# Kernel tuning notes

Hardware: AMD Instinct MI355X
Metric: run time of the kernel (lower is better)

Reference implementation:

```python
import jax, jax.numpy as jnp
import numpy as np

D_K = 64

def setup_inputs() -> dict:
    key = jax.random.key(0)
    k1, k2, k3 = jax.random.split(key, 3)
    shape = (4, 16, 2048, D_K)  # [batch, heads, seq, d_k]
    return {
        "q": jax.random.normal(k1, shape, dtype=jnp.float32),
        "k": jax.random.normal(k2, shape, dtype=jnp.float32),
        "v": jax.random.normal(k3, shape, dtype=jnp.float32),
    }

def reference(q, k, v):
    # scores: [B, H, S, S] = Q K^T / sqrt(d_k)
    scale = 1.0 / jnp.sqrt(jnp.asarray(D_K, dtype=q.dtype))
    scores = jnp.einsum("bhqd,bhkd->bhqk", q, k) * scale
    attn = jax.nn.softmax(scores, axis=-1)
    out = jnp.einsum("bhqk,bhkd->bhqd", attn, v)
    return out
```

## Files before the change

### kernel.cpp

```cpp
#include <hip/hip_runtime.h>


#define S_LEN 2048
#define D_K 64
#define BQ 256
#define BK 64
#define NT (S_LEN / BK)
#define LST 68

typedef __attribute__((ext_vector_type(8))) _Float16 fragh;
typedef __attribute__((ext_vector_type(4))) _Float16 half4v;
typedef __attribute__((ext_vector_type(2))) _Float16 half2v;
typedef __attribute__((ext_vector_type(16))) float f32x16;
typedef __attribute__((ext_vector_type(2))) unsigned int uint2v;
typedef __attribute__((ext_vector_type(4))) unsigned int uint4v;

__device__ __forceinline__ half2v pkrtz(float a, float b) {
  return __builtin_bit_cast(half2v, __builtin_amdgcn_cvt_pkrtz(a, b));
}
__device__ __forceinline__ half4v pk4(float a, float b, float c, float d) {
  return __builtin_shufflevector(pkrtz(a, b), pkrtz(c, d), 0, 1, 2, 3);
}
__device__ __forceinline__ fragh ldfrag(const _Float16* p) {
  half4v lo = *(const half4v*)p;
  half4v hv = *(const half4v*)(p + 4);
  return __builtin_shufflevector(lo, hv, 0, 1, 2, 3, 4, 5, 6, 7);
}

__global__ __launch_bounds__(512, 2) void sdpa_kernel(
    const float* __restrict__ q, const float* __restrict__ k,
    const float* __restrict__ v, float* __restrict__ out) {
  __shared__ _Float16 Ks[2][BK][LST];
  __shared__ _Float16 Vs[2][D_K][LST];

  const int t = threadIdx.x;
  const int wave = t >> 6;
  const int lane = t & 63;
  const int ln = lane & 31;
  const int hi = lane >> 5;

  const int blk = blockIdx.x;
  const int bh = (blk & 7) * 8 + (blk >> 6);
  const int q0 = ((blk >> 3) & 7) * BQ;

  const float* qp = q + ((size_t)bh * S_LEN + q0 + wave * 32) * D_K;
  const float* kp = k + (size_t)bh * S_LEN * D_K;
  const float* vp = v + (size_t)bh * S_LEN * D_K;

  const float qs = 0.125f * 1.44269504088896340736f;

  fragh qf[4];
  #pragma unroll
  for (int ks = 0; ks < 4; ++ks) {
    const float* src = qp + ln * D_K + ks * 16 + hi * 8;
    float4 a = *(const float4*)src;
    float4 b = *(const float4*)(src + 4);
    half4v lo = pk4(a.x * qs, a.y * qs, a.z * qs, a.w * qs);
    half4v hv = pk4(b.x * qs, b.y * qs, b.z * qs, b.w * qs);
    qf[ks] = __builtin_shufflevector(lo, hv, 0, 1, 2, 3, 4, 5, 6, 7);
  }

  const int pr = t & 31;
  const int dg = t >> 5;

  float4 kpre[2], vpre[2];
  {
    #pragma unroll
    for (int i = 0; i < 2; ++i) kpre[i] = *(const float4*)(kp + i * 2048 + t * 4);
    const float* vs0 = vp + 2 * pr * D_K + dg * 4;
    vpre[0] = *(const float4*)(vs0);
    vpre[1] = *(const float4*)(vs0 + D_K);
  }

  f32x16 O[2];
  #pragma unroll
  for (int dt = 0; dt < 2; ++dt)
    #pragma unroll
    for (int r = 0; r < 16; ++r) O[dt][r] = 0.f;
  float lsum = 0.f;

  #pragma unroll 2
  for (int kt = 0; kt < NT; ++kt) {
    const int bb = kt & 1;

    #pragma unroll
    for (int i = 0; i < 2; ++i) {
      int e = i * 2048 + t * 4;
      *(half4v*)&Ks[bb][e >> 6][e & 63] =
          pk4(kpre[i].x, kpre[i].y, kpre[i].z, kpre[i].w);
    }
    {
      int vd = dg * 4, vc = 2 * pr;
      *(half2v*)&Vs[bb][vd + 0][vc] = pkrtz(vpre[0].x, vpre[1].x);
      *(half2v*)&Vs[bb][vd + 1][vc] = pkrtz(vpre[0].y, vpre[1].y);
      *(half2v*)&Vs[bb][vd + 2][vc] = pkrtz(vpre[0].z, vpre[1].z);
      *(half2v*)&Vs[bb][vd + 3][vc] = pkrtz(vpre[0].w, vpre[1].w);
    }
    if (kt + 1 < NT) {
      const float* kb = kp + (kt + 1) * (BK * D_K);
      const float* vb = vp + (kt + 1) * (BK * D_K);
      #pragma unroll
      for (int i = 0; i < 2; ++i) kpre[i] = *(const float4*)(kb + i * 2048 + t * 4);
      const float* vs0 = vb + 2 * pr * D_K + dg * 4;
      vpre[0] = *(const float4*)(vs0);
      vpre[1] = *(const float4*)(vs0 + D_K);
    }
    __syncthreads();

    f32x16 sx[2];
    #pragma unroll
    for (int kt32 = 0; kt32 < 2; ++kt32) {
      fragh kf[4];
      #pragma unroll
      for (int ks = 0; ks < 4; ++ks)
        kf[ks] = ldfrag(&Ks[bb][kt32 * 32 + ln][ks * 16 + hi * 8]);
      f32x16 s;
      #pragma unroll
      for (int r = 0; r < 16; ++r) s[r] = 0.f;
      __builtin_amdgcn_s_setprio(1);
      #pragma unroll
      for (int ks = 0; ks < 4; ++ks)
        s = __builtin_amdgcn_mfma_f32_32x32x16_f16(kf[ks], qf[ks], s, 0, 0, 0);
      __builtin_amdgcn_s_setprio(0);
      sx[kt32] = s;
    }

    #pragma unroll
    for (int kt32 = 0; kt32 < 2; ++kt32) {
      fragh vf[2][2];
      #pragma unroll
      for (int ks16 = 0; ks16 < 2; ++ks16)
        #pragma unroll
        for (int dt = 0; dt < 2; ++dt)
          vf[ks16][dt] =
              ldfrag(&Vs[bb][dt * 32 + ln][kt32 * 32 + ks16 * 16 + hi * 8]);

      float p[16];
      #pragma unroll
      for (int r = 0; r < 16; ++r) p[r] = __builtin_amdgcn_exp2f(sx[kt32][r]);
      float t0 = (p[0] + p[1]) + (p[2] + p[3]);
      float t1 = (p[4] + p[5]) + (p[6] + p[7]);
      float t2 = (p[8] + p[9]) + (p[10] + p[11]);
      float t3 = (p[12] + p[13]) + (p[14] + p[15]);
      lsum += (t0 + t1) + (t2 + t3);

      unsigned w[8];
      #pragma unroll
      for (int i2 = 0; i2 < 8; ++i2)
        w[i2] = __builtin_bit_cast(unsigned, pkrtz(p[2 * i2], p[2 * i2 + 1]));
      uint2v a0 = __builtin_amdgcn_permlane32_swap(w[0], w[2], false, false);
      uint2v a1 = __builtin_amdgcn_permlane32_swap(w[1], w[3], false, false);
      uint2v a2 = __builtin_amdgcn_permlane32_swap(w[4], w[6], false, false);
      uint2v a3 = __builtin_amdgcn_permlane32_swap(w[5], w[7], false, false);
      uint4v f0 = {a0.x, a1.x, a0.y, a1.y};
      uint4v f1 = {a2.x, a3.x, a2.y, a3.y};
      fragh pf0 = __builtin_bit_cast(fragh, f0);
      fragh pf1 = __builtin_bit_cast(fragh, f1);

      __builtin_amdgcn_s_setprio(1);
      #pragma unroll
      for (int dt = 0; dt < 2; ++dt) {
        O[dt] = __builtin_amdgcn_mfma_f32_32x32x16_f16(vf[0][dt], pf0,
                                                       O[dt], 0, 0, 0);
        O[dt] = __builtin_amdgcn_mfma_f32_32x32x16_f16(vf[1][dt], pf1,
                                                       O[dt], 0, 0, 0);
      }
      __builtin_amdgcn_s_setprio(0);
    }
  }

  {
    float l = lsum + __shfl_xor(lsum, 32, 64);
    float inv = __builtin_amdgcn_rcpf(l);
    float* ob = out + ((size_t)bh * S_LEN + q0 + wave * 32 + ln) * D_K;
    #pragma unroll
    for (int dt = 0; dt < 2; ++dt) {
      #pragma unroll
      for (int g = 0; g < 4; ++g) {
        float4 o4;
        o4.x = O[dt][4 * g + 0] * inv;
        o4.y = O[dt][4 * g + 1] * inv;
        o4.z = O[dt][4 * g + 2] * inv;
        o4.w = O[dt][4 * g + 3] * inv;
        *(float4*)&ob[dt * 32 + g * 8 + hi * 4] = o4;
      }
    }
  }
}

extern "C" void kernel_launch(void* const* d_in, const int* in_sizes, int n_in,
                              void* d_out, int out_size, void* d_ws, size_t ws_size,
                              hipStream_t stream) {
  const float* q = (const float*)d_in[0];
  const float* k = (const float*)d_in[1];
  const float* v = (const float*)d_in[2];
  float* out = (float*)d_out;
  dim3 grid((S_LEN / BQ) * 64);
  dim3 block(512);
  sdpa_kernel<<<grid, block, 0, stream>>>(q, k, v, out);
}
```

Measured before the change: 191.9 us.

## Software-pipeline PV MFMA one tile behind QK with triple-buffered V

```diff
diff --git a/kernel.cpp b/kernel.cpp
--- a/kernel.cpp
+++ b/kernel.cpp
@@ -31,7 +31,7 @@
     const float* __restrict__ q, const float* __restrict__ k,
     const float* __restrict__ v, float* __restrict__ out) {
   __shared__ _Float16 Ks[2][BK][LST];
-  __shared__ _Float16 Vs[2][D_K][LST];
+  __shared__ _Float16 Vs[3][D_K][LST];
 
   const int t = threadIdx.x;
   const int wave = t >> 6;
@@ -79,7 +79,14 @@
     for (int r = 0; r < 16; ++r) O[dt][r] = 0.f;
   float lsum = 0.f;
 
-  #pragma unroll 2
+  fragh pz;
+  #pragma unroll
+  for (int j = 0; j < 8; ++j) pz[j] = (_Float16)0.f;
+  fragh pp00 = pz, pp01 = pz, pp10 = pz, pp11 = pz;
+
+  int vt = 0;
+  int pvt = 2;
+
   for (int kt = 0; kt < NT; ++kt) {
     const int bb = kt & 1;
 
@@ -91,10 +98,10 @@
     }
     {
       int vd = dg * 4, vc = 2 * pr;
-      *(half2v*)&Vs[bb][vd + 0][vc] = pkrtz(vpre[0].x, vpre[1].x);
-      *(half2v*)&Vs[bb][vd + 1][vc] = pkrtz(vpre[0].y, vpre[1].y);
-      *(half2v*)&Vs[bb][vd + 2][vc] = pkrtz(vpre[0].z, vpre[1].z);
-      *(half2v*)&Vs[bb][vd + 3][vc] = pkrtz(vpre[0].w, vpre[1].w);
+      *(half2v*)&Vs[vt][vd + 0][vc] = pkrtz(vpre[0].x, vpre[1].x);
+      *(half2v*)&Vs[vt][vd + 1][vc] = pkrtz(vpre[0].y, vpre[1].y);
+      *(half2v*)&Vs[vt][vd + 2][vc] = pkrtz(vpre[0].z, vpre[1].z);
+      *(half2v*)&Vs[vt][vd + 3][vc] = pkrtz(vpre[0].w, vpre[1].w);
     }
     if (kt + 1 < NT) {
       const float* kb = kp + (kt + 1) * (BK * D_K);
@@ -107,13 +114,12 @@
     }
     __syncthreads();
 
-    f32x16 sx[2];
-    #pragma unroll
-    for (int kt32 = 0; kt32 < 2; ++kt32) {
+    f32x16 sx0, sx1;
+    {
       fragh kf[4];
       #pragma unroll
       for (int ks = 0; ks < 4; ++ks)
-        kf[ks] = ldfrag(&Ks[bb][kt32 * 32 + ln][ks * 16 + hi * 8]);
+        kf[ks] = ldfrag(&Ks[bb][0 * 32 + ln][ks * 16 + hi * 8]);
       f32x16 s;
       #pragma unroll
       for (int r = 0; r < 16; ++r) s[r] = 0.f;
@@ -122,28 +128,34 @@
       for (int ks = 0; ks < 4; ++ks)
         s = __builtin_amdgcn_mfma_f32_32x32x16_f16(kf[ks], qf[ks], s, 0, 0, 0);
       __builtin_amdgcn_s_setprio(0);
-      sx[kt32] = s;
-    }
-
-    #pragma unroll
-    for (int kt32 = 0; kt32 < 2; ++kt32) {
-      fragh vf[2][2];
-      #pragma unroll
-      for (int ks16 = 0; ks16 < 2; ++ks16)
-        #pragma unroll
-        for (int dt = 0; dt < 2; ++dt)
-          vf[ks16][dt] =
-              ldfrag(&Vs[bb][dt * 32 + ln][kt32 * 32 + ks16 * 16 + hi * 8]);
-
+      sx0 = s;
+    }
+    {
+      fragh kf[4];
+      #pragma unroll
+      for (int ks = 0; ks < 4; ++ks)
+        kf[ks] = ldfrag(&Ks[bb][1 * 32 + ln][ks * 16 + hi * 8]);
+      f32x16 s;
+      #pragma unroll
+      for (int r = 0; r < 16; ++r) s[r] = 0.f;
+      __builtin_amdgcn_s_setprio(1);
+      #pragma unroll
+      for (int ks = 0; ks < 4; ++ks)
+        s = __builtin_amdgcn_mfma_f32_32x32x16_f16(kf[ks], qf[ks], s, 0, 0, 0);
+      __builtin_amdgcn_s_setprio(0);
+      sx1 = s;
+    }
+
+    fragh pn00, pn01, pn10, pn11;
+    {
       float p[16];
       #pragma unroll
-      for (int r = 0; r < 16; ++r) p[r] = __builtin_amdgcn_exp2f(sx[kt32][r]);
+      for (int r = 0; r < 16; ++r) p[r] = __builtin_amdgcn_exp2f(sx0[r]);
       float t0 = (p[0] + p[1]) + (p[2] + p[3]);
       float t1 = (p[4] + p[5]) + (p[6] + p[7]);
       float t2 = (p[8] + p[9]) + (p[10] + p[11]);
       float t3 = (p[12] + p[13]) + (p[14] + p[15]);
       lsum += (t0 + t1) + (t2 + t3);
-
       unsigned w[8];
       #pragma unroll
       for (int i2 = 0; i2 < 8; ++i2)
@@ -154,18 +166,81 @@
       uint2v a3 = __builtin_amdgcn_permlane32_swap(w[5], w[7], false, false);
       uint4v f0 = {a0.x, a1.x, a0.y, a1.y};
       uint4v f1 = {a2.x, a3.x, a2.y, a3.y};
-      fragh pf0 = __builtin_bit_cast(fragh, f0);
-      fragh pf1 = __builtin_bit_cast(fragh, f1);
-
-      __builtin_amdgcn_s_setprio(1);
-      #pragma unroll
-      for (int dt = 0; dt < 2; ++dt) {
-        O[dt] = __builtin_amdgcn_mfma_f32_32x32x16_f16(vf[0][dt], pf0,
-                                                       O[dt], 0, 0, 0);
-        O[dt] = __builtin_amdgcn_mfma_f32_32x32x16_f16(vf[1][dt], pf1,
-                                                       O[dt], 0, 0, 0);
-      }
-      __builtin_amdgcn_s_setprio(0);
+      pn00 = __builtin_bit_cast(fragh, f0);
+      pn01 = __builtin_bit_cast(fragh, f1);
+    }
+    if (kt > 0) {
+      fragh vfa[2], vfb[2];
+      #pragma unroll
+      for (int dt = 0; dt < 2; ++dt) {
+        vfa[dt] = ldfrag(&Vs[pvt][dt * 32 + ln][0 * 32 + 0 + hi * 8]);
+        vfb[dt] = ldfrag(&Vs[pvt][dt * 32 + ln][0 * 32 + 16 + hi * 8]);
+      }
+      __builtin_amdgcn_s_setprio(1);
+      #pragma unroll
+      for (int dt = 0; dt < 2; ++dt) {
+        O[dt] = __builtin_amdgcn_mfma_f32_32x32x16_f16(vfa[dt], pp00, O[dt], 0, 0, 0);
+        O[dt] = __builtin_amdgcn_mfma_f32_32x32x16_f16(vfb[dt], pp01, O[dt], 0, 0, 0);
+      }
+      __builtin_amdgcn_s_setprio(0);
+    }
+    {
+      float p[16];
+      #pragma unroll
+      for (int r = 0; r < 16; ++r) p[r] = __builtin_amdgcn_exp2f(sx1[r]);
+      float t0 = (p[0] + p[1]) + (p[2] + p[3]);
+      float t1 = (p[4] + p[5]) + (p[6] + p[7]);
+      float t2 = (p[8] + p[9]) + (p[10] + p[11]);
+      float t3 = (p[12] + p[13]) + (p[14] + p[15]);
+      lsum += (t0 + t1) + (t2 + t3);
+      unsigned w[8];
+      #pragma unroll
+      for (int i2 = 0; i2 < 8; ++i2)
+        w[i2] = __builtin_bit_cast(unsigned, pkrtz(p[2 * i2], p[2 * i2 + 1]));
+      uint2v a0 = __builtin_amdgcn_permlane32_swap(w[0], w[2], false, false);
+      uint2v a1 = __builtin_amdgcn_permlane32_swap(w[1], w[3], false, false);
+      uint2v a2 = __builtin_amdgcn_permlane32_swap(w[4], w[6], false, false);
+      uint2v a3 = __builtin_amdgcn_permlane32_swap(w[5], w[7], false, false);
+      uint4v f0 = {a0.x, a1.x, a0.y, a1.y};
+      uint4v f1 = {a2.x, a3.x, a2.y, a3.y};
+      pn10 = __builtin_bit_cast(fragh, f0);
+      pn11 = __builtin_bit_cast(fragh, f1);
+    }
+    if (kt > 0) {
+      fragh vfa[2], vfb[2];
+      #pragma unroll
+      for (int dt = 0; dt < 2; ++dt) {
+        vfa[dt] = ldfrag(&Vs[pvt][dt * 32 + ln][1 * 32 + 0 + hi * 8]);
+        vfb[dt] = ldfrag(&Vs[pvt][dt * 32 + ln][1 * 32 + 16 + hi * 8]);
+      }
+      __builtin_amdgcn_s_setprio(1);
+      #pragma unroll
+      for (int dt = 0; dt < 2; ++dt) {
+        O[dt] = __builtin_amdgcn_mfma_f32_32x32x16_f16(vfa[dt], pp10, O[dt], 0, 0, 0);
+        O[dt] = __builtin_amdgcn_mfma_f32_32x32x16_f16(vfb[dt], pp11, O[dt], 0, 0, 0);
+      }
+      __builtin_amdgcn_s_setprio(0);
+    }
+
+    pp00 = pn00; pp01 = pn01; pp10 = pn10; pp11 = pn11;
+    pvt = vt;
+    vt = (vt == 2) ? 0 : vt + 1;
+  }
+
+  #pragma unroll
+  for (int j = 0; j < 2; ++j) {
+    fragh vfa[2], vfb[2];
+    #pragma unroll
+    for (int dt = 0; dt < 2; ++dt) {
+      vfa[dt] = ldfrag(&Vs[pvt][dt * 32 + ln][j * 32 + 0 + hi * 8]);
+      vfb[dt] = ldfrag(&Vs[pvt][dt * 32 + ln][j * 32 + 16 + hi * 8]);
+    }
+    fragh p0 = j ? pp10 : pp00;
+    fragh p1 = j ? pp11 : pp01;
+    #pragma unroll
+    for (int dt = 0; dt < 2; ++dt) {
+      O[dt] = __builtin_amdgcn_mfma_f32_32x32x16_f16(vfa[dt], p0, O[dt], 0, 0, 0);
+      O[dt] = __builtin_amdgcn_mfma_f32_32x32x16_f16(vfb[dt], p1, O[dt], 0, 0, 0);
     }
   }
 
```

Result: slower. 198.1 us (+3.2%).
